# Kernel tuning notes

Hardware: AMD Instinct MI355X
Metric: run time of the kernel (lower is better)

Reference implementation:

```python
import jax, jax.numpy as jnp
import numpy as np
from functools import partial

H = 51  # hidden size hard-coded in the module
B = 1024
T = 1024


def setup_inputs() -> dict:
    key = jax.random.key(0)
    ks = jax.random.split(key, 12)
    scale = 1.0 / np.sqrt(H)
    p = lambda k, shape: (jax.random.normal(k, shape, dtype=jnp.float32) * scale)
    return {
        "input": jax.random.normal(ks[0], (B, T), dtype=jnp.float32),
        # layer 1: LSTMCell(1, 51)
        "W_ih1": p(ks[1], (4 * H, 1)),
        "W_hh1": p(ks[2], (4 * H, H)),
        "b_ih1": p(ks[3], (4 * H,)),
        "b_hh1": p(ks[4], (4 * H,)),
        # layer 2: LSTMCell(51, 51)
        "W_ih2": p(ks[5], (4 * H, H)),
        "W_hh2": p(ks[6], (4 * H, H)),
        "b_ih2": p(ks[7], (4 * H,)),
        "b_hh2": p(ks[8], (4 * H,)),
        # Linear(51, 1)
        "W_lin": p(ks[9], (1, H)),
        "b_lin": p(ks[10], (1,)),
    }


def _lstm_cell(x, h, c, W_ih, W_hh, b_ih, b_hh):
    # PyTorch LSTMCell gate order: i, f, g, o
    gates = x @ W_ih.T + h @ W_hh.T + b_ih + b_hh  # [B, 4H]
    i, f, g, o = jnp.split(gates, 4, axis=-1)
    i = jax.nn.sigmoid(i)
    f = jax.nn.sigmoid(f)
    g = jnp.tanh(g)
    o = jax.nn.sigmoid(o)
    c_new = f * c + i * g
    h_new = o * jnp.tanh(c_new)
    return h_new, c_new


def reference(input, W_ih1, W_hh1, b_ih1, b_hh1, W_ih2, W_hh2, b_ih2, b_hh2, W_lin, b_lin):
    Bv = input.shape[0]
    dt = input.dtype
    init = (
        jnp.zeros((Bv, H), dt),  # h1
        jnp.zeros((Bv, H), dt),  # c1
        jnp.zeros((Bv, H), dt),  # h2
        jnp.zeros((Bv, H), dt),  # c2
    )

    def step(carry, x_t):  # x_t: [B, 1]
        h1, c1, h2, c2 = carry
        h1, c1 = _lstm_cell(x_t, h1, c1, W_ih1, W_hh1, b_ih1, b_hh1)
        h2, c2 = _lstm_cell(h1, h2, c2, W_ih2, W_hh2, b_ih2, b_hh2)
        y = h2 @ W_lin.T + b_lin  # [B, 1]
        return (h1, c1, h2, c2), y[:, 0]

    xs = input.T[:, :, None]  # [T, B, 1]
    _, ys = jax.lax.scan(step, init, xs)  # ys: [T, B]
    return ys.T  # [B, T]
```

## Files before the change

### kernel.cpp

```cpp
#include <hip/hip_runtime.h>


#define H     51
#define NROW  204
#define TLEN  1024
#define BPB   16
#define NTHR  896
#define NBLK  64
#define KPAD  88

#define LOG2E  1.442695041f
#define LOG2E2 2.885390082f

typedef __attribute__((ext_vector_type(8))) _Float16 half8;
typedef __attribute__((ext_vector_type(4))) float f4;

__device__ __forceinline__ float frcp(float x) { return __builtin_amdgcn_rcpf(x); }
#if __has_builtin(__builtin_amdgcn_exp2f)
__device__ __forceinline__ float ex2(float x) { return __builtin_amdgcn_exp2f(x); }
#else
__device__ __forceinline__ float ex2(float x) { return __expf(x * 0.6931471806f); }
#endif

__device__ __forceinline__ half8 lds8h(const _Float16* p) {
    return *(const half8*)__builtin_assume_aligned(p, 16);
}

#define MFMA(ACC, A, B) \
    ACC = __builtin_amdgcn_mfma_f32_16x16x32_f16((A), (B), (ACC), 0, 0, 0)

__device__ __forceinline__ half8 load_wfrag(const float* __restrict__ W,
                                            int tile, int kt, int q, int mcol)
{
    half8 hf;
    const int prow = tile * 16 + mcol;
    const float sc = ((prow & 3) == 2) ? LOG2E2 : LOG2E;
#pragma unroll
    for (int j = 0; j < 8; ++j) {
        const int kk = kt * 32 + q * 8 + j;
        float v = 0.0f;
        if (prow < NROW && kk < H) {
            const int srow = (prow & 3) * H + (prow >> 2);
            v = W[srow * H + kk];
        }
        hf[j] = (_Float16)(v * sc);
    }
    return hf;
}

__device__ __forceinline__ float cell(float a_i, float a_f, float b_g,
                                      float d_o, float* c)
{
    const float e_i = ex2(-a_i);
    const float e_f = ex2(-a_f);
    const float Eg  = ex2(b_g);
    const float f   = frcp(1.0f + e_f);
    const float ig  = (Eg - 1.0f) * frcp((1.0f + e_i) * (Eg + 1.0f));
    const float cn  = fmaf(f, *c, ig);
    *c = cn;
    const float Ec  = ex2(cn * LOG2E2);
    const float e_o = ex2(-d_o);
    return (Ec - 1.0f) * frcp((Ec + 1.0f) * (1.0f + e_o));
}

__global__
__attribute__((amdgpu_flat_work_group_size(NTHR, NTHR), amdgpu_waves_per_eu(4, 4)))
void lstm2_kernel(const float* __restrict__ input,
                  const float* __restrict__ W_ih1, const float* __restrict__ W_hh1,
                  const float* __restrict__ b_ih1, const float* __restrict__ b_hh1,
                  const float* __restrict__ W_ih2, const float* __restrict__ W_hh2,
                  const float* __restrict__ b_ih2, const float* __restrict__ b_hh2,
                  const float* __restrict__ W_lin, const float* __restrict__ b_lin,
                  float* __restrict__ out)
{
    const int tid  = threadIdx.x;
    const int w    = tid >> 6;
    const int lane = tid & 63;
    const int q    = lane >> 4;
    const int mcol = lane & 15;
    const int b0   = blockIdx.x * BPB;

    const bool tile_wave = (w < 13);
    const bool y_wave    = (w == 13);

    __shared__ __align__(16) _Float16 hb[2][2][BPB][KPAD];

    {
        _Float16* hz = &hb[0][0][0][0];
        for (int i = tid; i < 2 * 2 * BPB * KPAD; i += NTHR) hz[i] = (_Float16)0.0f;
    }

    half8 A1[2], Ai[2], Ah[2];
    f4 bb1, bb2, wxv;
    float c1 = 0.0f, c2 = 0.0f;
    const int t = w;
    const int u = 4 * t + q;

    if (tile_wave) {
#pragma unroll
        for (int kt = 0; kt < 2; ++kt) {
            A1[kt] = load_wfrag(W_hh1, t, kt, q, mcol);
            Ai[kt] = load_wfrag(W_ih2, t, kt, q, mcol);
            Ah[kt] = load_wfrag(W_hh2, t, kt, q, mcol);
        }
#pragma unroll
        for (int j = 0; j < 4; ++j) {
            const bool v = (u < H);
            const float sc = (j == 2) ? LOG2E2 : LOG2E;
            bb1[j] = v ? sc * (b_ih1[j * H + u] + b_hh1[j * H + u]) : 0.0f;
            bb2[j] = v ? sc * (b_ih2[j * H + u] + b_hh2[j * H + u]) : 0.0f;
            wxv[j] = v ? sc * W_ih1[j * H + u] : 0.0f;
        }
    }

    float wl[16];
    if (y_wave) {
#pragma unroll
        for (int i = 0; i < 16; ++i) {
            const int r = q * 16 + i;
            wl[i] = (r < H) ? W_lin[r] : 0.0f;
        }
    }
    const float blin = b_lin[0];

    float xcur = input[(size_t)(b0 + mcol) * TLEN + 0];

    __syncthreads();

#define STEP(KK, RB, WB, L2EN, YEN)                                            \
do {                                                                           \
    const int k_  = (KK);                                                      \
    const int kn_ = (k_ + 1 < TLEN) ? (k_ + 1) : (TLEN - 1);                   \
    const float xnext_ = input[(size_t)(b0 + mcol) * TLEN + kn_];              \
    if (tile_wave) {                                                           \
        half8 B1a = lds8h(&hb[RB][0][mcol][q * 8]);                            \
        half8 B1b = lds8h(&hb[RB][0][mcol][32 + q * 8]);                       \
        f4 g1;                                                                 \
        g1[0] = fmaf(wxv[0], xcur, bb1[0]);                                    \
        g1[1] = fmaf(wxv[1], xcur, bb1[1]);                                    \
        g1[2] = fmaf(wxv[2], xcur, bb1[2]);                                    \
        g1[3] = fmaf(wxv[3], xcur, bb1[3]);                                    \
        MFMA(g1, A1[0], B1a);  MFMA(g1, A1[1], B1b);                           \
                                                         \
        const float h1n = cell(g1[0], g1[1], g1[2], g1[3], &c1);               \
        hb[WB][0][mcol][u] = (_Float16)h1n;                                    \
        if (L2EN) {                                                            \
            half8 B2a = lds8h(&hb[RB][1][mcol][q * 8]);                        \
            half8 B2b = lds8h(&hb[RB][1][mcol][32 + q * 8]);                   \
            f4 g2 = bb2;                                                       \
            MFMA(g2, Ai[0], B1a);  MFMA(g2, Ai[1], B1b);                       \
            MFMA(g2, Ah[0], B2a);  MFMA(g2, Ah[1], B2b);                       \
                                                       \
            const float h2n = cell(g2[0], g2[1], g2[2], g2[3], &c2);           \
            hb[WB][1][mcol][u] = (_Float16)h2n;                                \
        }                                                                      \
    } else if (y_wave && (YEN)) {                                              \
               \
        half8 y0 = lds8h(&hb[RB][1][mcol][q * 16]);                            \
        half8 y1 = lds8h(&hb[RB][1][mcol][q * 16 + 8]);                        \
        float yp = 0.0f;                                                       \
        _Pragma("unroll")                                                      \
        for (int i = 0; i < 8; ++i) {                                          \
            yp += wl[i]     * (float)y0[i];                                    \
            yp += wl[i + 8] * (float)y1[i];                                    \
        }                                                                      \
        yp += __shfl_xor(yp, 16);                                              \
        yp += __shfl_xor(yp, 32);                                              \
        if (q == 0) out[(size_t)(b0 + mcol) * TLEN + (k_ - 2)] = yp + blin;    \
    }                                                                          \
    __syncthreads();                                                           \
    xcur = xnext_;                                                             \
} while (0)

    STEP(0, 1, 0, 0, 0);
    STEP(1, 0, 1, 1, 0);
    for (int k = 2; k < TLEN; k += 2) {
        STEP(k, 1, 0, 1, 1);
        STEP(k + 1, 0, 1, 1, 1);
    }
    STEP(TLEN, 1, 0, 1, 1);
#undef STEP

    if (y_wave) {
        half8 y0 = lds8h(&hb[0][1][mcol][q * 16]);
        half8 y1 = lds8h(&hb[0][1][mcol][q * 16 + 8]);
        float yp = 0.0f;
#pragma unroll
        for (int i = 0; i < 8; ++i) {
            yp += wl[i]     * (float)y0[i];
            yp += wl[i + 8] * (float)y1[i];
        }
        yp += __shfl_xor(yp, 16);
        yp += __shfl_xor(yp, 32);
        if (q == 0) out[(size_t)(b0 + mcol) * TLEN + (TLEN - 1)] = yp + blin;
    }
}

extern "C" void kernel_launch(void* const* d_in, const int* in_sizes, int n_in,
                              void* d_out, int out_size, void* d_ws, size_t ws_size,
                              hipStream_t stream)
{
    const float* input = (const float*)d_in[0];
    const float* W_ih1 = (const float*)d_in[1];
    const float* W_hh1 = (const float*)d_in[2];
    const float* b_ih1 = (const float*)d_in[3];
    const float* b_hh1 = (const float*)d_in[4];
    const float* W_ih2 = (const float*)d_in[5];
    const float* W_hh2 = (const float*)d_in[6];
    const float* b_ih2 = (const float*)d_in[7];
    const float* b_hh2 = (const float*)d_in[8];
    const float* W_lin = (const float*)d_in[9];
    const float* b_lin = (const float*)d_in[10];

    float* out = (float*)d_out;

    hipLaunchKernelGGL(lstm2_kernel, dim3(NBLK), dim3(NTHR), 0, stream,
                       input, W_ih1, W_hh1, b_ih1, b_hh1,
                       W_ih2, W_hh2, b_ih2, b_hh2, W_lin, b_lin,
                       out);
}
```

Before: 781.5 us.

## Assign two gate tiles per wave with permuted hidden layout, halving workgroup size

The workgroup shrinks from 14 to 8 waves. Each of 7 compute waves now handles two 16-row gate tiles (13 tiles total), with independent MFMA chains and cell evaluations interleaved in each step. The hidden-state positions in LDS are permuted via posu/ipos so the stores from the two tiles land in a different pattern, likely to reduce bank conflicts, and weight fragments and linear weights are loaded with the matching inverse permutation. The aim is to cut per-step barrier cost across fewer waves and overlap the work of the two tiles, at the cost of more registers per wave and a longer serial path per wave.

```diff
diff --git a/kernel.cpp b/kernel.cpp
--- a/kernel.cpp
+++ b/kernel.cpp
@@ -5,7 +5,7 @@
 #define NROW  204
 #define TLEN  1024
 #define BPB   16
-#define NTHR  896
+#define NTHR  512
 #define NBLK  64
 #define KPAD  88
 
@@ -22,6 +22,13 @@
 __device__ __forceinline__ float ex2(float x) { return __expf(x * 0.6931471806f); }
 #endif
 
+__device__ __forceinline__ int posu(int u) {
+    return (u & ~7) | ((u & 3) << 1) | ((u >> 2) & 1);
+}
+__device__ __forceinline__ int ipos(int p) {
+    return (p & ~7) | ((p & 1) << 2) | ((p >> 1) & 3);
+}
+
 __device__ __forceinline__ half8 lds8h(const _Float16* p) {
     return *(const half8*)__builtin_assume_aligned(p, 16);
 }
@@ -37,7 +44,7 @@
     const float sc = ((prow & 3) == 2) ? LOG2E2 : LOG2E;
 #pragma unroll
     for (int j = 0; j < 8; ++j) {
-        const int kk = kt * 32 + q * 8 + j;
+        const int kk = ipos(kt * 32 + q * 8 + j);
         float v = 0.0f;
         if (prow < NROW && kk < H) {
             const int srow = (prow & 3) * H + (prow >> 2);
@@ -64,7 +71,7 @@
 }
 
 __global__
-__attribute__((amdgpu_flat_work_group_size(NTHR, NTHR), amdgpu_waves_per_eu(4, 4)))
+__attribute__((amdgpu_flat_work_group_size(NTHR, NTHR), amdgpu_waves_per_eu(2, 2)))
 void lstm2_kernel(const float* __restrict__ input,
                   const float* __restrict__ W_ih1, const float* __restrict__ W_hh1,
                   const float* __restrict__ b_ih1, const float* __restrict__ b_hh1,
@@ -80,8 +87,8 @@
     const int mcol = lane & 15;
     const int b0   = blockIdx.x * BPB;
 
-    const bool tile_wave = (w < 13);
-    const bool y_wave    = (w == 13);
+    const bool tile_wave = (w < 7);
+    const bool y_wave    = (w == 7);
 
     __shared__ __align__(16) _Float16 hb[2][2][BPB][KPAD];
 
@@ -90,26 +97,38 @@
         for (int i = tid; i < 2 * 2 * BPB * KPAD; i += NTHR) hz[i] = (_Float16)0.0f;
     }
 
-    half8 A1[2], Ai[2], Ah[2];
-    f4 bb1, bb2, wxv;
-    float c1 = 0.0f, c2 = 0.0f;
-    const int t = w;
-    const int u = 4 * t + q;
+    const int t0 = w;
+    const int t1 = 7 + w;
+    const bool s2 = tile_wave && (t1 < 13);
+
+    half8 A1[2][2], Ai[2][2], Ah[2][2];
+    f4 bb1[2], bb2[2], wxv[2];
+    float c1_0 = 0.0f, c2_0 = 0.0f, c1_1 = 0.0f, c2_1 = 0.0f;
+    int   wp0 = 0, wp1 = 0;
 
     if (tile_wave) {
-#pragma unroll
-        for (int kt = 0; kt < 2; ++kt) {
-            A1[kt] = load_wfrag(W_hh1, t, kt, q, mcol);
-            Ai[kt] = load_wfrag(W_ih2, t, kt, q, mcol);
-            Ah[kt] = load_wfrag(W_hh2, t, kt, q, mcol);
-        }
-#pragma unroll
-        for (int j = 0; j < 4; ++j) {
-            const bool v = (u < H);
-            const float sc = (j == 2) ? LOG2E2 : LOG2E;
-            bb1[j] = v ? sc * (b_ih1[j * H + u] + b_hh1[j * H + u]) : 0.0f;
-            bb2[j] = v ? sc * (b_ih2[j * H + u] + b_hh2[j * H + u]) : 0.0f;
-            wxv[j] = v ? sc * W_ih1[j * H + u] : 0.0f;
+        const int tt[2] = {t0, t1};
+#pragma unroll
+        for (int s = 0; s < 2; ++s) {
+            const int t = tt[s];
+            const int u = 4 * t + q;
+            if (s == 0) wp0 = posu(u); else wp1 = posu(u);
+            if (t < 13) {
+#pragma unroll
+                for (int kt = 0; kt < 2; ++kt) {
+                    A1[s][kt] = load_wfrag(W_hh1, t, kt, q, mcol);
+                    Ai[s][kt] = load_wfrag(W_ih2, t, kt, q, mcol);
+                    Ah[s][kt] = load_wfrag(W_hh2, t, kt, q, mcol);
+                }
+#pragma unroll
+                for (int j = 0; j < 4; ++j) {
+                    const bool v = (u < H);
+                    const float sc = (j == 2) ? LOG2E2 : LOG2E;
+                    bb1[s][j] = v ? sc * (b_ih1[j * H + u] + b_hh1[j * H + u]) : 0.0f;
+                    bb2[s][j] = v ? sc * (b_ih2[j * H + u] + b_hh2[j * H + u]) : 0.0f;
+                    wxv[s][j] = v ? sc * W_ih1[j * H + u] : 0.0f;
+                }
+            }
         }
     }
 
@@ -117,7 +136,7 @@
     if (y_wave) {
 #pragma unroll
         for (int i = 0; i < 16; ++i) {
-            const int r = q * 16 + i;
+            const int r = ipos(q * 16 + i);
             wl[i] = (r < H) ? W_lin[r] : 0.0f;
         }
     }
@@ -135,24 +154,39 @@
     if (tile_wave) {                                                           \
         half8 B1a = lds8h(&hb[RB][0][mcol][q * 8]);                            \
         half8 B1b = lds8h(&hb[RB][0][mcol][32 + q * 8]);                       \
-        f4 g1;                                                                 \
-        g1[0] = fmaf(wxv[0], xcur, bb1[0]);                                    \
-        g1[1] = fmaf(wxv[1], xcur, bb1[1]);                                    \
-        g1[2] = fmaf(wxv[2], xcur, bb1[2]);                                    \
-        g1[3] = fmaf(wxv[3], xcur, bb1[3]);                                    \
-        MFMA(g1, A1[0], B1a);  MFMA(g1, A1[1], B1b);                           \
-                                                         \
-        const float h1n = cell(g1[0], g1[1], g1[2], g1[3], &c1);               \
-        hb[WB][0][mcol][u] = (_Float16)h1n;                                    \
+        f4 g1_0;                                                               \
+        g1_0[0] = fmaf(wxv[0][0], xcur, bb1[0][0]);                            \
+        g1_0[1] = fmaf(wxv[0][1], xcur, bb1[0][1]);                            \
+        g1_0[2] = fmaf(wxv[0][2], xcur, bb1[0][2]);                            \
+        g1_0[3] = fmaf(wxv[0][3], xcur, bb1[0][3]);                            \
+        MFMA(g1_0, A1[0][0], B1a);  MFMA(g1_0, A1[0][1], B1b);                 \
+        if (s2) {                                                              \
+            f4 g1_1;                                                           \
+            g1_1[0] = fmaf(wxv[1][0], xcur, bb1[1][0]);                        \
+            g1_1[1] = fmaf(wxv[1][1], xcur, bb1[1][1]);                        \
+            g1_1[2] = fmaf(wxv[1][2], xcur, bb1[1][2]);                        \
+            g1_1[3] = fmaf(wxv[1][3], xcur, bb1[1][3]);                        \
+            MFMA(g1_1, A1[1][0], B1a);  MFMA(g1_1, A1[1][1], B1b);             \
+            const float h1n1 = cell(g1_1[0], g1_1[1], g1_1[2], g1_1[3], &c1_1);\
+            hb[WB][0][mcol][wp1] = (_Float16)h1n1;                             \
+        }                                                                      \
+        const float h1n0 = cell(g1_0[0], g1_0[1], g1_0[2], g1_0[3], &c1_0);    \
+        hb[WB][0][mcol][wp0] = (_Float16)h1n0;                                 \
         if (L2EN) {                                                            \
             half8 B2a = lds8h(&hb[RB][1][mcol][q * 8]);                        \
             half8 B2b = lds8h(&hb[RB][1][mcol][32 + q * 8]);                   \
-            f4 g2 = bb2;                                                       \
-            MFMA(g2, Ai[0], B1a);  MFMA(g2, Ai[1], B1b);                       \
-            MFMA(g2, Ah[0], B2a);  MFMA(g2, Ah[1], B2b);                       \
-                                                       \
-            const float h2n = cell(g2[0], g2[1], g2[2], g2[3], &c2);           \
-            hb[WB][1][mcol][u] = (_Float16)h2n;                                \
+            f4 g2_0 = bb2[0];                                                  \
+            MFMA(g2_0, Ai[0][0], B1a);  MFMA(g2_0, Ai[0][1], B1b);             \
+            MFMA(g2_0, Ah[0][0], B2a);  MFMA(g2_0, Ah[0][1], B2b);             \
+            if (s2) {                                                          \
+                f4 g2_1 = bb2[1];                                              \
+                MFMA(g2_1, Ai[1][0], B1a);  MFMA(g2_1, Ai[1][1], B1b);         \
+                MFMA(g2_1, Ah[1][0], B2a);  MFMA(g2_1, Ah[1][1], B2b);         \
+                const float h2n1 = cell(g2_1[0], g2_1[1], g2_1[2], g2_1[3], &c2_1); \
+                hb[WB][1][mcol][wp1] = (_Float16)h2n1;                         \
+            }                                                                  \
+            const float h2n0 = cell(g2_0[0], g2_0[1], g2_0[2], g2_0[3], &c2_0);\
+            hb[WB][1][mcol][wp0] = (_Float16)h2n0;                             \
         }                                                                      \
     } else if (y_wave && (YEN)) {                                              \
                \
```

Measured after the change: 860.3 us. 10.1% more time.
